# Kernel tuning notes

Hardware: AMD Instinct MI355X
Metric: run time of the kernel (lower is better)

Reference implementation:

```python
import jax, jax.numpy as jnp
import numpy as np

NUM_USER = 100000
NUM_ENT = 100000
NUM_REL = 60
NUM_ITEM = 20000
ITEM_NUM_IN_KG = 20000
DIM = 64
N_NEIGHBOR = 8
N_ITER = 2
BATCH = 16384


def setup_inputs() -> dict:
    key = jax.random.key(0)
    ks = jax.random.split(key, 10)
    return {
        "u": jax.random.randint(ks[0], (BATCH,), 0, NUM_USER),
        "v": jax.random.randint(ks[1], (BATCH,), 0, NUM_ITEM),
        "usr_emb": jax.random.normal(ks[2], (NUM_USER, DIM), jnp.float32),
        "item_emb": jax.random.normal(ks[3], (NUM_ITEM, DIM), jnp.float32),
        "ent_emb": jax.random.normal(ks[4], (NUM_ENT + 1, DIM), jnp.float32),
        "rel_emb": jax.random.normal(ks[5], (NUM_REL + 1, DIM), jnp.float32),
        "W": jax.random.normal(ks[6], (DIM, DIM), jnp.float32) / np.sqrt(DIM),
        "b": jax.random.normal(ks[7], (DIM,), jnp.float32) * 0.01,
        "adj_ent": jax.random.randint(ks[8], (NUM_ENT + 1, N_NEIGHBOR), 0, NUM_ENT + 1),
        "adj_rel": jax.random.randint(ks[9], (NUM_ENT + 1, N_NEIGHBOR), 0, NUM_REL + 1),
    }


def reference(u, v, usr_emb, item_emb, ent_emb, rel_emb, W, b, adj_ent, adj_rel):
    B = u.shape[0]
    ue = usr_emb[u]  # [B, D]

    # hop-0 indices: items not in the KG map to the padding entity for neighbor lookup
    v_clip = jnp.where(v >= ITEM_NUM_IN_KG, NUM_ENT, v)
    ents = [v_clip[:, None]]  # [B, 1]
    rels = []
    for h in range(N_ITER):
        rels.append(adj_rel[ents[h]].reshape(B, -1))  # [B, 8**(h+1)]
        ents.append(adj_ent[ents[h]].reshape(B, -1))

    # hop-0 embedding uses the ORIGINAL v via the item table (entities[0][:] = v)
    ev = [item_emb[v[:, None]]] + [ent_emb[e] for e in ents[1:]]  # each [B, m, D]
    rv = [rel_emb[r] for r in rels]

    for i in range(N_ITER):
        act = jnp.tanh if i == N_ITER - 1 else jax.nn.sigmoid
        nxt = []
        for hop in range(N_ITER - i):
            sv = ev[hop]  # [B, m, D]
            m = sv.shape[1]
            nv = ev[hop + 1].reshape(B, m, N_NEIGHBOR, DIM)
            nr = rv[hop].reshape(B, m, N_NEIGHBOR, DIM)
            # user-relation attention over the 8 sampled neighbors
            scores = jnp.einsum("bd,bmnd->bmn", ue, nr)
            wgt = jax.nn.softmax(scores, axis=-1)
            agg = jnp.einsum("bmn,bmnd->bmd", wgt, nv)
            out = (sv + agg) @ W.T + b  # 'sum' aggregator
            nxt.append(act(out))
        ev = nxt

    item_vec = ev[0].reshape(B, DIM)
    return jax.nn.sigmoid(jnp.sum(ue * item_vec, axis=1))  # [B]
```

## Files before the change

kernel.cpp:

```cpp
#include <hip/hip_runtime.h>
#include <hip/hip_fp16.h>


namespace {

constexpr int kDim      = 64;
constexpr int kNN       = 8;
constexpr int kNumEnt   = 100000;
constexpr int kItemInKG = 20000;
constexpr int kElems    = 8;
constexpr int kRelChunks = 976;
constexpr int kP        = 68;
constexpr size_t kEntHalfBytes = (size_t)(kNumEnt + 1) * kDim * sizeof(__half);

typedef _Float16 f16x4 __attribute__((ext_vector_type(4)));
typedef _Float16 f16x8 __attribute__((ext_vector_type(8)));
typedef float    f32x4 __attribute__((ext_vector_type(4)));

__device__ __forceinline__ float fast_sigmoid(float x) {
  return 1.0f / (1.0f + __expf(-x));
}
__device__ __forceinline__ float fast_tanh(float x) {
  return 2.0f / (1.0f + __expf(-2.0f * x)) - 1.0f;
}
__device__ __forceinline__ float readlane_f(float v, int lane) {
  return __int_as_float(__builtin_amdgcn_readlane(__float_as_int(v), lane));
}
__device__ __forceinline__ f16x8 join8(f16x4 lo, f16x4 hi) {
  return __builtin_shufflevector(lo, hi, 0, 1, 2, 3, 4, 5, 6, 7);
}
__device__ __forceinline__ f16x4 cvt4(float4 f) {
  f16x4 h;
  h[0] = (_Float16)f.x; h[1] = (_Float16)f.y;
  h[2] = (_Float16)f.z; h[3] = (_Float16)f.w;
  return h;
}

__global__ void __launch_bounds__(256)
conv_kernel(const float* __restrict__ src, __half2* __restrict__ dst, int n4) {
  const int i = blockIdx.x * 256 + threadIdx.x;
  if (i < n4) {
    const float4 f = reinterpret_cast<const float4*>(src)[i];
    dst[2 * i + 0] = __floats2half2_rn(f.x, f.y);
    dst[2 * i + 1] = __floats2half2_rn(f.z, f.w);
  }
}

template <bool HALF>
__global__ void __launch_bounds__(kElems * 64)
__attribute__((amdgpu_waves_per_eu(4)))
kgcn_kernel(const int* __restrict__ u, const int* __restrict__ v,
            const float* __restrict__ usr_emb, const float* __restrict__ item_emb,
            const float* __restrict__ ent_emb, const __half* __restrict__ ent_h,
            const float* __restrict__ rel_emb,
            const float* __restrict__ W, const float* __restrict__ bias,
            const int* __restrict__ adj_ent, const int* __restrict__ adj_rel,
            float* __restrict__ out)
{
  const int tid = threadIdx.x;
  const int wv  = tid >> 6;
  const int ln  = tid & 63;
  const int lq  = ln & 15;
  const int lg  = ln >> 4;
  const int b   = blockIdx.x * kElems + wv;

  __shared__ __align__(16) _Float16 s_wh[kDim * kP];
  __shared__ __align__(16) _Float16 s_relh[kDim * kP];
  __shared__ __align__(16) _Float16 s_ueh[kElems * kDim];
  __shared__ __align__(16) _Float16 s_pre[72 * kP];
  __shared__ __align__(16) _Float16 s_h[72 * kP];
  __shared__ float s_w2[kElems][kDim];

  const float4* W4 = reinterpret_cast<const float4*>(W);
  const float4* R4 = reinterpret_cast<const float4*>(rel_emb);
  const float4 wst0 = W4[tid];
  const float4 wst1 = W4[512 + tid];
  const float4 rst0 = R4[tid];
  const float4 rst1 = (512 + tid < kRelChunks) ? R4[512 + tid]
                                               : make_float4(0.f, 0.f, 0.f, 0.f);

  const int bs    = __builtin_amdgcn_readfirstlane(b);
  const int uid_s = u[bs];
  const int vid_s = v[bs];
  const int e0s   = (vid_s >= kItemInKG) ? kNumEnt : vid_s;

  const float ue  = usr_emb[(size_t)uid_s * kDim + ln];
  const float ev0 = item_emb[(size_t)vid_s * kDim + ln];

  int e1s[kNN];
  {
    const int* __restrict__ a0 = adj_ent + (size_t)e0s * kNN;
    #pragma unroll
    for (int m = 0; m < kNN; ++m) e1s[m] = a0[m];
  }
  int e2s[kDim];
  #pragma unroll
  for (int m = 0; m < kNN; ++m) {
    const int* __restrict__ am = adj_ent + (size_t)e1s[m] * kNN;
    #pragma unroll
    for (int n = 0; n < kNN; ++n) e2s[m * kNN + n] = am[n];
  }
  int r1v = 0;
  if (ln < kNN) r1v = adj_rel[(size_t)e0s * kNN + ln];
  int parent = e1s[0];
  #pragma unroll
  for (int m = 1; m < kNN; ++m)
    parent = ((ln >> 3) == m) ? e1s[m] : parent;
  const int r2v = adj_rel[(size_t)parent * kNN + (ln & 7)];

  {
    int id = tid, row = id >> 4, c4 = (id & 15) << 2;
    *reinterpret_cast<f16x4*>(&s_wh[row * kP + c4]) = cvt4(wst0);
    *reinterpret_cast<f16x4*>(&s_relh[row * kP + c4]) = cvt4(rst0);
    id = 512 + tid; row = id >> 4; c4 = (id & 15) << 2;
    *reinterpret_cast<f16x4*>(&s_wh[row * kP + c4]) = cvt4(wst1);
    *reinterpret_cast<f16x4*>(&s_relh[row * kP + c4]) = cvt4(rst1);
  }
  s_ueh[wv * kDim + ln] = (_Float16)ue;

  float ev1r[kNN];
  #pragma unroll
  for (int m = 0; m < kNN; ++m) {
    const size_t row = (size_t)e1s[m] * kDim + ln;
    ev1r[m] = HALF ? __half2float(ent_h[row]) : ent_emb[row];
  }

  unsigned short g16[kDim];
  if constexpr (HALF) {
    const unsigned short* eh = reinterpret_cast<const unsigned short*>(ent_h);
    #pragma unroll
    for (int i = 0; i < kDim; ++i)
      g16[i] = eh[(size_t)e2s[i] * kDim + ln];
  }

  __syncthreads();

  f16x8 Au[2];
  #pragma unroll
  for (int s = 0; s < 2; ++s) {
    const _Float16* p = &s_ueh[wv * kDim + s * 32 + lg * 4];
    Au[s] = join8(*reinterpret_cast<const f16x4*>(p),
                  *reinterpret_cast<const f16x4*>(p + 16));
  }
  f32x4 ts[4];
  #pragma unroll
  for (int tt = 0; tt < 4; ++tt) {
    ts[tt] = f32x4{0.f, 0.f, 0.f, 0.f};
    #pragma unroll
    for (int s = 0; s < 2; ++s) {
      const _Float16* p = &s_relh[(tt * 16 + lq) * kP + s * 32 + lg * 4];
      const f16x8 Rf = join8(*reinterpret_cast<const f16x4*>(p),
                             *reinterpret_cast<const f16x4*>(p + 16));
      ts[tt] = __builtin_amdgcn_mfma_f32_16x16x32_f16(Au[s], Rf, ts[tt],
                                                      0, 0, 0);
    }
  }
  auto t_lookup = [&](int r) -> float {
    const int sl = r & 15;
    const float c0 = __shfl(ts[0][0], sl, 64);
    const float c1 = __shfl(ts[1][0], sl, 64);
    const float c2 = __shfl(ts[2][0], sl, 64);
    const float c3 = __shfl(ts[3][0], sl, 64);
    const float ab = (r & 16) ? c1 : c0;
    const float cd = (r & 16) ? c3 : c2;
    return (r & 32) ? cd : ab;
  };

  {
    const float s2 = t_lookup(r2v);
    float mx = s2;
    #pragma unroll
    for (int m = 1; m <= 4; m <<= 1) mx = fmaxf(mx, __shfl_xor(mx, m, 64));
    const float e = __expf(s2 - mx);
    float sm = e;
    #pragma unroll
    for (int m = 1; m <= 4; m <<= 1) sm += __shfl_xor(sm, m, 64);
    s_w2[wv][ln] = e / sm;
  }
  float w0v;
  {
    const float s0 = t_lookup(r1v);
    float mx = s0;
    #pragma unroll
    for (int m = 1; m <= 4; m <<= 1) mx = fmaxf(mx, __shfl_xor(mx, m, 64));
    w0v = __expf(s0 - mx);
    float sm = w0v;
    #pragma unroll
    for (int m = 1; m <= 4; m <<= 1) sm += __shfl_xor(sm, m, 64);
    w0v /= sm;
  }

  if constexpr (HALF) {
    #pragma unroll
    for (int i = 0; i < kDim; ++i) asm volatile("" : "+v"(g16[i]));
  }

  {
    float agg = 0.f;
    #pragma unroll
    for (int n = 0; n < kNN; ++n)
      agg = fmaf(readlane_f(w0v, n), ev1r[n], agg);
    s_pre[(wv * 9 + 0) * kP + ln] = (_Float16)(ev0 + agg);
  }
  if constexpr (HALF) {
    #pragma unroll
    for (int m = 0; m < kNN; ++m) {
      float acc = 0.f;
      #pragma unroll
      for (int n = 0; n < kNN; ++n) {
        const _Float16 hv =
            __builtin_bit_cast(_Float16, g16[m * kNN + n]);
        acc = fmaf((float)hv, s_w2[wv][m * kNN + n], acc);
      }
      s_pre[(wv * 9 + 1 + m) * kP + ln] = (_Float16)(ev1r[m] + acc);
    }
  } else {
    #pragma unroll 2
    for (int m = 0; m < kNN; ++m) {
      float acc = 0.f;
      #pragma unroll
      for (int n = 0; n < kNN; ++n) {
        const size_t row = (size_t)e2s[m * kNN + n] * kDim + ln;
        acc = fmaf(s_w2[wv][m * kNN + n], ent_emb[row], acc);
      }
      s_pre[(wv * 9 + 1 + m) * kP + ln] = (_Float16)(ev1r[m] + acc);
    }
  }

  float bcol[4];
  #pragma unroll
  for (int tt = 0; tt < 4; ++tt) bcol[tt] = bias[tt * 16 + lq];

  f16x8 Bf[8];
  #pragma unroll
  for (int tt = 0; tt < 4; ++tt) {
    #pragma unroll
    for (int s = 0; s < 2; ++s) {
      const _Float16* p = &s_wh[(tt * 16 + lq) * kP + s * 32 + lg * 4];
      Bf[tt * 2 + s] = join8(*reinterpret_cast<const f16x4*>(p),
                             *reinterpret_cast<const f16x4*>(p + 16));
    }
  }

  const int arow = wv * 9 + (lq < 9 ? lq : 8);
  f16x8 Af[2];
  #pragma unroll
  for (int s = 0; s < 2; ++s) {
    const _Float16* p = &s_pre[arow * kP + s * 32 + lg * 4];
    Af[s] = join8(*reinterpret_cast<const f16x4*>(p),
                  *reinterpret_cast<const f16x4*>(p + 16));
  }
  f32x4 acc[4];
  #pragma unroll
  for (int tt = 0; tt < 4; ++tt) acc[tt] = f32x4{0.f, 0.f, 0.f, 0.f};
  #pragma unroll
  for (int tt = 0; tt < 4; ++tt)
    #pragma unroll
    for (int s = 0; s < 2; ++s)
      acc[tt] = __builtin_amdgcn_mfma_f32_16x16x32_f16(Af[s], Bf[tt * 2 + s],
                                                       acc[tt], 0, 0, 0);

  #pragma unroll
  for (int tt = 0; tt < 4; ++tt) {
    #pragma unroll
    for (int r = 0; r < 4; ++r) {
      const int vec = lg * 4 + r;
      if (vec < 9)
        s_h[(wv * 9 + vec) * kP + tt * 16 + lq] =
            (_Float16)fast_sigmoid(acc[tt][r] + bcol[tt]);
    }
  }

  {
    float pre = (float)s_h[(wv * 9 + 0) * kP + ln];
    #pragma unroll
    for (int n = 0; n < kNN; ++n)
      pre = fmaf(readlane_f(w0v, n), (float)s_h[(wv * 9 + 1 + n) * kP + ln],
                 pre);
    s_pre[(wv * 9 + 0) * kP + ln] = (_Float16)pre;
  }

  f16x8 Ff[2];
  #pragma unroll
  for (int s = 0; s < 2; ++s) {
    const _Float16* p = &s_pre[(wv * 9 + 0) * kP + s * 32 + lg * 4];
    Ff[s] = join8(*reinterpret_cast<const f16x4*>(p),
                  *reinterpret_cast<const f16x4*>(p + 16));
  }
  f32x4 fa[4];
  #pragma unroll
  for (int tt = 0; tt < 4; ++tt) fa[tt] = f32x4{0.f, 0.f, 0.f, 0.f};
  #pragma unroll
  for (int tt = 0; tt < 4; ++tt)
    #pragma unroll
    for (int s = 0; s < 2; ++s)
      fa[tt] = __builtin_amdgcn_mfma_f32_16x16x32_f16(Ff[s], Bf[tt * 2 + s],
                                                      fa[tt], 0, 0, 0);

  {
    float fown = fa[0][0], bown = bcol[0];
    if (lg == 1) { fown = fa[1][0]; bown = bcol[1]; }
    if (lg == 2) { fown = fa[2][0]; bown = bcol[2]; }
    if (lg == 3) { fown = fa[3][0]; bown = bcol[3]; }
    float part = fast_tanh(fown + bown) * ue;
    #pragma unroll
    for (int off = 32; off > 0; off >>= 1)
      part += __shfl_xor(part, off, 64);
    if (ln == 0) out[b] = fast_sigmoid(part);
  }
}

}

extern "C" void kernel_launch(void* const* d_in, const int* in_sizes, int n_in,
                              void* d_out, int out_size, void* d_ws, size_t ws_size,
                              hipStream_t stream) {
  const int*   u        = (const int*)d_in[0];
  const int*   v        = (const int*)d_in[1];
  const float* usr_emb  = (const float*)d_in[2];
  const float* item_emb = (const float*)d_in[3];
  const float* ent_emb  = (const float*)d_in[4];
  const float* rel_emb  = (const float*)d_in[5];
  const float* W        = (const float*)d_in[6];
  const float* bias     = (const float*)d_in[7];
  const int*   adj_ent  = (const int*)d_in[8];
  const int*   adj_rel  = (const int*)d_in[9];
  float*       out      = (float*)d_out;

  const int B = in_sizes[0];
  dim3 grid(B / kElems), block(kElems * 64);

  const bool use_half = (ws_size >= kEntHalfBytes);
  if (use_half) {
    __half* ent_h = (__half*)d_ws;
    const int n4 = (kNumEnt + 1) * kDim / 4;
    hipLaunchKernelGGL(conv_kernel, dim3((n4 + 255) / 256), dim3(256), 0,
                       stream, ent_emb, (__half2*)ent_h, n4);
    hipLaunchKernelGGL((kgcn_kernel<true>), grid, block, 0, stream,
                       u, v, usr_emb, item_emb, ent_emb, ent_h, rel_emb, W,
                       bias, adj_ent, adj_rel, out);
  } else {
    hipLaunchKernelGGL((kgcn_kernel<false>), grid, block, 0, stream,
                       u, v, usr_emb, item_emb, ent_emb, (const __half*)d_ws,
                       rel_emb, W, bias, adj_ent, adj_rel, out);
  }
}
```

Measured before the change: 52.26 us.

## Process two batch elements per wave with software-pipelined gathers

Each wave now handles two batch elements, and the grid is halved. Index and embedding gathers for the second element are issued while the first element's attention and MLP math runs, so memory latency is hidden and the per-block staging of W and relation tables is amortized. The cost is many more live registers (two 64-entry gather arrays), which may cut occupancy or cause spills, and fewer blocks in flight.

Measured after the change: 103.6 us. 98.3% more time.

```diff
diff --git a/kernel.cpp b/kernel.cpp
--- a/kernel.cpp
+++ b/kernel.cpp
@@ -9,6 +9,7 @@
 constexpr int kNumEnt   = 100000;
 constexpr int kItemInKG = 20000;
 constexpr int kElems    = 8;
+constexpr int kEPW      = 2;
 constexpr int kRelChunks = 976;
 constexpr int kP        = 68;
 constexpr size_t kEntHalfBytes = (size_t)(kNumEnt + 1) * kDim * sizeof(__half);
@@ -62,7 +63,8 @@
   const int ln  = tid & 63;
   const int lq  = ln & 15;
   const int lg  = ln >> 4;
-  const int b   = blockIdx.x * kElems + wv;
+  const int b0  = blockIdx.x * (kElems * kEPW) + wv;
+  const int b1  = b0 + kElems;
 
   __shared__ __align__(16) _Float16 s_wh[kDim * kP];
   __shared__ __align__(16) _Float16 s_relh[kDim * kP];
@@ -79,34 +81,44 @@
   const float4 rst1 = (512 + tid < kRelChunks) ? R4[512 + tid]
                                                : make_float4(0.f, 0.f, 0.f, 0.f);
 
-  const int bs    = __builtin_amdgcn_readfirstlane(b);
-  const int uid_s = u[bs];
-  const int vid_s = v[bs];
-  const int e0s   = (vid_s >= kItemInKG) ? kNumEnt : vid_s;
-
-  const float ue  = usr_emb[(size_t)uid_s * kDim + ln];
-  const float ev0 = item_emb[(size_t)vid_s * kDim + ln];
-
-  int e1s[kNN];
-  {
-    const int* __restrict__ a0 = adj_ent + (size_t)e0s * kNN;
-    #pragma unroll
-    for (int m = 0; m < kNN; ++m) e1s[m] = a0[m];
-  }
-  int e2s[kDim];
+  const int bs0   = __builtin_amdgcn_readfirstlane(b0);
+  const int uid0  = u[bs0];
+  const int vid0  = v[bs0];
+  const int e0s0  = (vid0 >= kItemInKG) ? kNumEnt : vid0;
+  const float ue0  = usr_emb[(size_t)uid0 * kDim + ln];
+  const float ev00 = item_emb[(size_t)vid0 * kDim + ln];
+
+  int e1s0[kNN];
+  {
+    const int* __restrict__ a0 = adj_ent + (size_t)e0s0 * kNN;
+    #pragma unroll
+    for (int m = 0; m < kNN; ++m) e1s0[m] = a0[m];
+  }
+  int e2s0[kDim];
   #pragma unroll
   for (int m = 0; m < kNN; ++m) {
-    const int* __restrict__ am = adj_ent + (size_t)e1s[m] * kNN;
-    #pragma unroll
-    for (int n = 0; n < kNN; ++n) e2s[m * kNN + n] = am[n];
-  }
-  int r1v = 0;
-  if (ln < kNN) r1v = adj_rel[(size_t)e0s * kNN + ln];
-  int parent = e1s[0];
+    const int* __restrict__ am = adj_ent + (size_t)e1s0[m] * kNN;
+    #pragma unroll
+    for (int n = 0; n < kNN; ++n) e2s0[m * kNN + n] = am[n];
+  }
+  int r1v0 = 0;
+  if (ln < kNN) r1v0 = adj_rel[(size_t)e0s0 * kNN + ln];
+  int parent0 = e1s0[0];
   #pragma unroll
   for (int m = 1; m < kNN; ++m)
-    parent = ((ln >> 3) == m) ? e1s[m] : parent;
-  const int r2v = adj_rel[(size_t)parent * kNN + (ln & 7)];
+    parent0 = ((ln >> 3) == m) ? e1s0[m] : parent0;
+  const int r2v0 = adj_rel[(size_t)parent0 * kNN + (ln & 7)];
+
+  const int bs1   = __builtin_amdgcn_readfirstlane(b1);
+  const int uid1  = u[bs1];
+  const int vid1  = v[bs1];
+  const int e0s1  = (vid1 >= kItemInKG) ? kNumEnt : vid1;
+  int e1s1[kNN];
+  {
+    const int* __restrict__ a1 = adj_ent + (size_t)e0s1 * kNN;
+    #pragma unroll
+    for (int m = 0; m < kNN; ++m) e1s1[m] = a1[m];
+  }
 
   {
     int id = tid, row = id >> 4, c4 = (id & 15) << 2;
@@ -116,91 +128,123 @@
     *reinterpret_cast<f16x4*>(&s_wh[row * kP + c4]) = cvt4(wst1);
     *reinterpret_cast<f16x4*>(&s_relh[row * kP + c4]) = cvt4(rst1);
   }
-  s_ueh[wv * kDim + ln] = (_Float16)ue;
-
-  float ev1r[kNN];
+  s_ueh[wv * kDim + ln] = (_Float16)ue0;
+
+  float ev1r0[kNN];
   #pragma unroll
   for (int m = 0; m < kNN; ++m) {
-    const size_t row = (size_t)e1s[m] * kDim + ln;
-    ev1r[m] = HALF ? __half2float(ent_h[row]) : ent_emb[row];
-  }
-
-  unsigned short g16[kDim];
+    const size_t row = (size_t)e1s0[m] * kDim + ln;
+    ev1r0[m] = HALF ? __half2float(ent_h[row]) : ent_emb[row];
+  }
+  unsigned short g16_0[kDim];
   if constexpr (HALF) {
     const unsigned short* eh = reinterpret_cast<const unsigned short*>(ent_h);
     #pragma unroll
     for (int i = 0; i < kDim; ++i)
-      g16[i] = eh[(size_t)e2s[i] * kDim + ln];
-  }
+      g16_0[i] = eh[(size_t)e2s0[i] * kDim + ln];
+  }
+
+  int e2s1[kDim];
+  #pragma unroll
+  for (int m = 0; m < kNN; ++m) {
+    const int* __restrict__ am = adj_ent + (size_t)e1s1[m] * kNN;
+    #pragma unroll
+    for (int n = 0; n < kNN; ++n) e2s1[m * kNN + n] = am[n];
+  }
+  int r1v1 = 0;
+  if (ln < kNN) r1v1 = adj_rel[(size_t)e0s1 * kNN + ln];
+  int parent1 = e1s1[0];
+  #pragma unroll
+  for (int m = 1; m < kNN; ++m)
+    parent1 = ((ln >> 3) == m) ? e1s1[m] : parent1;
+  const int r2v1 = adj_rel[(size_t)parent1 * kNN + (ln & 7)];
 
   __syncthreads();
 
-  f16x8 Au[2];
-  #pragma unroll
-  for (int s = 0; s < 2; ++s) {
-    const _Float16* p = &s_ueh[wv * kDim + s * 32 + lg * 4];
-    Au[s] = join8(*reinterpret_cast<const f16x4*>(p),
-                  *reinterpret_cast<const f16x4*>(p + 16));
-  }
-  f32x4 ts[4];
-  #pragma unroll
-  for (int tt = 0; tt < 4; ++tt) {
-    ts[tt] = f32x4{0.f, 0.f, 0.f, 0.f};
-    #pragma unroll
-    for (int s = 0; s < 2; ++s) {
-      const _Float16* p = &s_relh[(tt * 16 + lq) * kP + s * 32 + lg * 4];
-      const f16x8 Rf = join8(*reinterpret_cast<const f16x4*>(p),
-                             *reinterpret_cast<const f16x4*>(p + 16));
-      ts[tt] = __builtin_amdgcn_mfma_f32_16x16x32_f16(Au[s], Rf, ts[tt],
-                                                      0, 0, 0);
-    }
-  }
-  auto t_lookup = [&](int r) -> float {
-    const int sl = r & 15;
-    const float c0 = __shfl(ts[0][0], sl, 64);
-    const float c1 = __shfl(ts[1][0], sl, 64);
-    const float c2 = __shfl(ts[2][0], sl, 64);
-    const float c3 = __shfl(ts[3][0], sl, 64);
-    const float ab = (r & 16) ? c1 : c0;
-    const float cd = (r & 16) ? c3 : c2;
-    return (r & 32) ? cd : ab;
-  };
-
-  {
-    const float s2 = t_lookup(r2v);
-    float mx = s2;
-    #pragma unroll
-    for (int m = 1; m <= 4; m <<= 1) mx = fmaxf(mx, __shfl_xor(mx, m, 64));
-    const float e = __expf(s2 - mx);
-    float sm = e;
-    #pragma unroll
-    for (int m = 1; m <= 4; m <<= 1) sm += __shfl_xor(sm, m, 64);
-    s_w2[wv][ln] = e / sm;
-  }
-  float w0v;
-  {
-    const float s0 = t_lookup(r1v);
-    float mx = s0;
-    #pragma unroll
-    for (int m = 1; m <= 4; m <<= 1) mx = fmaxf(mx, __shfl_xor(mx, m, 64));
-    w0v = __expf(s0 - mx);
-    float sm = w0v;
-    #pragma unroll
-    for (int m = 1; m <= 4; m <<= 1) sm += __shfl_xor(sm, m, 64);
-    w0v /= sm;
+  float w0v0, w2v_unused0;
+  {
+    f16x8 Au[2];
+    #pragma unroll
+    for (int s = 0; s < 2; ++s) {
+      const _Float16* p = &s_ueh[wv * kDim + s * 32 + lg * 4];
+      Au[s] = join8(*reinterpret_cast<const f16x4*>(p),
+                    *reinterpret_cast<const f16x4*>(p + 16));
+    }
+    f32x4 ts[4];
+    #pragma unroll
+    for (int tt = 0; tt < 4; ++tt) {
+      ts[tt] = f32x4{0.f, 0.f, 0.f, 0.f};
+      #pragma unroll
+      for (int s = 0; s < 2; ++s) {
+        const _Float16* p = &s_relh[(tt * 16 + lq) * kP + s * 32 + lg * 4];
+        const f16x8 Rf = join8(*reinterpret_cast<const f16x4*>(p),
+                               *reinterpret_cast<const f16x4*>(p + 16));
+        ts[tt] = __builtin_amdgcn_mfma_f32_16x16x32_f16(Au[s], Rf, ts[tt],
+                                                        0, 0, 0);
+      }
+    }
+    auto t_lookup = [&](int r) -> float {
+      const int sl = r & 15;
+      const float c0 = __shfl(ts[0][0], sl, 64);
+      const float c1 = __shfl(ts[1][0], sl, 64);
+      const float c2 = __shfl(ts[2][0], sl, 64);
+      const float c3 = __shfl(ts[3][0], sl, 64);
+      const float ab = (r & 16) ? c1 : c0;
+      const float cd = (r & 16) ? c3 : c2;
+      return (r & 32) ? cd : ab;
+    };
+    {
+      const float s2 = t_lookup(r2v0);
+      float mx = s2;
+      #pragma unroll
+      for (int m = 1; m <= 4; m <<= 1) mx = fmaxf(mx, __shfl_xor(mx, m, 64));
+      const float e = __expf(s2 - mx);
+      float sm = e;
+      #pragma unroll
+      for (int m = 1; m <= 4; m <<= 1) sm += __shfl_xor(sm, m, 64);
+      s_w2[wv][ln] = e / sm;
+    }
+    {
+      const float s0 = t_lookup(r1v0);
+      float mx = s0;
+      #pragma unroll
+      for (int m = 1; m <= 4; m <<= 1) mx = fmaxf(mx, __shfl_xor(mx, m, 64));
+      w0v0 = __expf(s0 - mx);
+      float sm = w0v0;
+      #pragma unroll
+      for (int m = 1; m <= 4; m <<= 1) sm += __shfl_xor(sm, m, 64);
+      w0v0 /= sm;
+    }
+    (void)w2v_unused0;
   }
 
   if constexpr (HALF) {
     #pragma unroll
-    for (int i = 0; i < kDim; ++i) asm volatile("" : "+v"(g16[i]));
+    for (int i = 0; i < kDim; ++i) asm volatile("" : "+v"(g16_0[i]));
+  }
+
+  const float ue1  = usr_emb[(size_t)uid1 * kDim + ln];
+  const float ev01 = item_emb[(size_t)vid1 * kDim + ln];
+  float ev1r1[kNN];
+  #pragma unroll
+  for (int m = 0; m < kNN; ++m) {
+    const size_t row = (size_t)e1s1[m] * kDim + ln;
+    ev1r1[m] = HALF ? __half2float(ent_h[row]) : ent_emb[row];
+  }
+  unsigned short g16_1[kDim];
+  if constexpr (HALF) {
+    const unsigned short* eh = reinterpret_cast<const unsigned short*>(ent_h);
+    #pragma unroll
+    for (int i = 0; i < kDim; ++i)
+      g16_1[i] = eh[(size_t)e2s1[i] * kDim + ln];
   }
 
   {
     float agg = 0.f;
     #pragma unroll
     for (int n = 0; n < kNN; ++n)
-      agg = fmaf(readlane_f(w0v, n), ev1r[n], agg);
-    s_pre[(wv * 9 + 0) * kP + ln] = (_Float16)(ev0 + agg);
+      agg = fmaf(readlane_f(w0v0, n), ev1r0[n], agg);
+    s_pre[(wv * 9 + 0) * kP + ln] = (_Float16)(ev00 + agg);
   }
   if constexpr (HALF) {
     #pragma unroll
@@ -208,11 +252,10 @@
       float acc = 0.f;
       #pragma unroll
       for (int n = 0; n < kNN; ++n) {
-        const _Float16 hv =
-            __builtin_bit_cast(_Float16, g16[m * kNN + n]);
+        const _Float16 hv = __builtin_bit_cast(_Float16, g16_0[m * kNN + n]);
         acc = fmaf((float)hv, s_w2[wv][m * kNN + n], acc);
       }
-      s_pre[(wv * 9 + 1 + m) * kP + ln] = (_Float16)(ev1r[m] + acc);
+      s_pre[(wv * 9 + 1 + m) * kP + ln] = (_Float16)(ev1r0[m] + acc);
     }
   } else {
     #pragma unroll 2
@@ -220,17 +263,16 @@
       float acc = 0.f;
       #pragma unroll
       for (int n = 0; n < kNN; ++n) {
-        const size_t row = (size_t)e2s[m * kNN + n] * kDim + ln;
+        const size_t row = (size_t)e2s0[m * kNN + n] * kDim + ln;
         acc = fmaf(s_w2[wv][m * kNN + n], ent_emb[row], acc);
       }
-      s_pre[(wv * 9 + 1 + m) * kP + ln] = (_Float16)(ev1r[m] + acc);
+      s_pre[(wv * 9 + 1 + m) * kP + ln] = (_Float16)(ev1r0[m] + acc);
     }
   }
 
   float bcol[4];
   #pragma unroll
   for (int tt = 0; tt < 4; ++tt) bcol[tt] = bias[tt * 16 + lq];
-
   f16x8 Bf[8];
   #pragma unroll
   for (int tt = 0; tt < 4; ++tt) {
@@ -241,72 +283,223 @@
                              *reinterpret_cast<const f16x4*>(p + 16));
     }
   }
-
   const int arow = wv * 9 + (lq < 9 ? lq : 8);
-  f16x8 Af[2];
-  #pragma unroll
-  for (int s = 0; s < 2; ++s) {
-    const _Float16* p = &s_pre[arow * kP + s * 32 + lg * 4];
-    Af[s] = join8(*reinterpret_cast<const f16x4*>(p),
-                  *reinterpret_cast<const f16x4*>(p + 16));
-  }
-  f32x4 acc[4];
-  #pragma unroll
-  for (int tt = 0; tt < 4; ++tt) acc[tt] = f32x4{0.f, 0.f, 0.f, 0.f};
-  #pragma unroll
-  for (int tt = 0; tt < 4; ++tt)
-    #pragma unroll
-    for (int s = 0; s < 2; ++s)
-      acc[tt] = __builtin_amdgcn_mfma_f32_16x16x32_f16(Af[s], Bf[tt * 2 + s],
-                                                       acc[tt], 0, 0, 0);
-
-  #pragma unroll
-  for (int tt = 0; tt < 4; ++tt) {
-    #pragma unroll
-    for (int r = 0; r < 4; ++r) {
-      const int vec = lg * 4 + r;
-      if (vec < 9)
-        s_h[(wv * 9 + vec) * kP + tt * 16 + lq] =
-            (_Float16)fast_sigmoid(acc[tt][r] + bcol[tt]);
-    }
-  }
-
-  {
-    float pre = (float)s_h[(wv * 9 + 0) * kP + ln];
-    #pragma unroll
-    for (int n = 0; n < kNN; ++n)
-      pre = fmaf(readlane_f(w0v, n), (float)s_h[(wv * 9 + 1 + n) * kP + ln],
-                 pre);
-    s_pre[(wv * 9 + 0) * kP + ln] = (_Float16)pre;
-  }
-
-  f16x8 Ff[2];
-  #pragma unroll
-  for (int s = 0; s < 2; ++s) {
-    const _Float16* p = &s_pre[(wv * 9 + 0) * kP + s * 32 + lg * 4];
-    Ff[s] = join8(*reinterpret_cast<const f16x4*>(p),
-                  *reinterpret_cast<const f16x4*>(p + 16));
-  }
-  f32x4 fa[4];
-  #pragma unroll
-  for (int tt = 0; tt < 4; ++tt) fa[tt] = f32x4{0.f, 0.f, 0.f, 0.f};
-  #pragma unroll
-  for (int tt = 0; tt < 4; ++tt)
-    #pragma unroll
-    for (int s = 0; s < 2; ++s)
-      fa[tt] = __builtin_amdgcn_mfma_f32_16x16x32_f16(Ff[s], Bf[tt * 2 + s],
-                                                      fa[tt], 0, 0, 0);
-
-  {
+
+  {
+    f16x8 Af[2];
+    #pragma unroll
+    for (int s = 0; s < 2; ++s) {
+      const _Float16* p = &s_pre[arow * kP + s * 32 + lg * 4];
+      Af[s] = join8(*reinterpret_cast<const f16x4*>(p),
+                    *reinterpret_cast<const f16x4*>(p + 16));
+    }
+    f32x4 acc[4];
+    #pragma unroll
+    for (int tt = 0; tt < 4; ++tt) acc[tt] = f32x4{0.f, 0.f, 0.f, 0.f};
+    #pragma unroll
+    for (int tt = 0; tt < 4; ++tt)
+      #pragma unroll
+      for (int s = 0; s < 2; ++s)
+        acc[tt] = __builtin_amdgcn_mfma_f32_16x16x32_f16(Af[s], Bf[tt * 2 + s],
+                                                         acc[tt], 0, 0, 0);
+    #pragma unroll
+    for (int tt = 0; tt < 4; ++tt) {
+      #pragma unroll
+      for (int r = 0; r < 4; ++r) {
+        const int vec = lg * 4 + r;
+        if (vec < 9)
+          s_h[(wv * 9 + vec) * kP + tt * 16 + lq] =
+              (_Float16)fast_sigmoid(acc[tt][r] + bcol[tt]);
+      }
+    }
+    {
+      float pre = (float)s_h[(wv * 9 + 0) * kP + ln];
+      #pragma unroll
+      for (int n = 0; n < kNN; ++n)
+        pre = fmaf(readlane_f(w0v0, n),
+                   (float)s_h[(wv * 9 + 1 + n) * kP + ln], pre);
+      s_pre[(wv * 9 + 0) * kP + ln] = (_Float16)pre;
+    }
+    f16x8 Ff[2];
+    #pragma unroll
+    for (int s = 0; s < 2; ++s) {
+      const _Float16* p = &s_pre[(wv * 9 + 0) * kP + s * 32 + lg * 4];
+      Ff[s] = join8(*reinterpret_cast<const f16x4*>(p),
+                    *reinterpret_cast<const f16x4*>(p + 16));
+    }
+    f32x4 fa[4];
+    #pragma unroll
+    for (int tt = 0; tt < 4; ++tt) fa[tt] = f32x4{0.f, 0.f, 0.f, 0.f};
+    #pragma unroll
+    for (int tt = 0; tt < 4; ++tt)
+      #pragma unroll
+      for (int s = 0; s < 2; ++s)
+        fa[tt] = __builtin_amdgcn_mfma_f32_16x16x32_f16(Ff[s], Bf[tt * 2 + s],
+                                                        fa[tt], 0, 0, 0);
     float fown = fa[0][0], bown = bcol[0];
     if (lg == 1) { fown = fa[1][0]; bown = bcol[1]; }
     if (lg == 2) { fown = fa[2][0]; bown = bcol[2]; }
     if (lg == 3) { fown = fa[3][0]; bown = bcol[3]; }
-    float part = fast_tanh(fown + bown) * ue;
+    float part = fast_tanh(fown + bown) * ue0;
     #pragma unroll
     for (int off = 32; off > 0; off >>= 1)
       part += __shfl_xor(part, off, 64);
-    if (ln == 0) out[b] = fast_sigmoid(part);
+    if (ln == 0) out[b0] = fast_sigmoid(part);
+  }
+
+  s_ueh[wv * kDim + ln] = (_Float16)ue1;
+  float w0v1;
+  {
+    f16x8 Au[2];
+    #pragma unroll
+    for (int s = 0; s < 2; ++s) {
+      const _Float16* p = &s_ueh[wv * kDim + s * 32 + lg * 4];
+      Au[s] = join8(*reinterpret_cast<const f16x4*>(p),
+                    *reinterpret_cast<const f16x4*>(p + 16));
+    }
+    f32x4 ts[4];
+    #pragma unroll
+    for (int tt = 0; tt < 4; ++tt) {
+      ts[tt] = f32x4{0.f, 0.f, 0.f, 0.f};
+      #pragma unroll
+      for (int s = 0; s < 2; ++s) {
+        const _Float16* p = &s_relh[(tt * 16 + lq) * kP + s * 32 + lg * 4];
+        const f16x8 Rf = join8(*reinterpret_cast<const f16x4*>(p),
+                               *reinterpret_cast<const f16x4*>(p + 16));
+        ts[tt] = __builtin_amdgcn_mfma_f32_16x16x32_f16(Au[s], Rf, ts[tt],
+                                                        0, 0, 0);
+      }
+    }
+    auto t_lookup = [&](int r) -> float {
+      const int sl = r & 15;
+      const float c0 = __shfl(ts[0][0], sl, 64);
+      const float c1 = __shfl(ts[1][0], sl, 64);
+      const float c2 = __shfl(ts[2][0], sl, 64);
+      const float c3 = __shfl(ts[3][0], sl, 64);
+      const float ab = (r & 16) ? c1 : c0;
+      const float cd = (r & 16) ? c3 : c2;
+      return (r & 32) ? cd : ab;
+    };
+    {
+      const float s2 = t_lookup(r2v1);
+      float mx = s2;
+      #pragma unroll
+      for (int m = 1; m <= 4; m <<= 1) mx = fmaxf(mx, __shfl_xor(mx, m, 64));
+      const float e = __expf(s2 - mx);
+      float sm = e;
+      #pragma unroll
+      for (int m = 1; m <= 4; m <<= 1) sm += __shfl_xor(sm, m, 64);
+      s_w2[wv][ln] = e / sm;
+    }
+    {
+      const float s0 = t_lookup(r1v1);
+      float mx = s0;
+      #pragma unroll
+      for (int m = 1; m <= 4; m <<= 1) mx = fmaxf(mx, __shfl_xor(mx, m, 64));
+      w0v1 = __expf(s0 - mx);
+      float sm = w0v1;
+      #pragma unroll
+      for (int m = 1; m <= 4; m <<= 1) sm += __shfl_xor(sm, m, 64);
+      w0v1 /= sm;
+    }
+  }
+
+  if constexpr (HALF) {
+    #pragma unroll
+    for (int i = 0; i < kDim; ++i) asm volatile("" : "+v"(g16_1[i]));
+  }
+
+  {
+    float agg = 0.f;
+    #pragma unroll
+    for (int n = 0; n < kNN; ++n)
+      agg = fmaf(readlane_f(w0v1, n), ev1r1[n], agg);
+    s_pre[(wv * 9 + 0) * kP + ln] = (_Float16)(ev01 + agg);
+  }
+  if constexpr (HALF) {
+    #pragma unroll
+    for (int m = 0; m < kNN; ++m) {
+      float acc = 0.f;
+      #pragma unroll
+      for (int n = 0; n < kNN; ++n) {
+        const _Float16 hv = __builtin_bit_cast(_Float16, g16_1[m * kNN + n]);
+        acc = fmaf((float)hv, s_w2[wv][m * kNN + n], acc);
+      }
+      s_pre[(wv * 9 + 1 + m) * kP + ln] = (_Float16)(ev1r1[m] + acc);
+    }
+  } else {
+    #pragma unroll 2
+    for (int m = 0; m < kNN; ++m) {
+      float acc = 0.f;
+      #pragma unroll
+      for (int n = 0; n < kNN; ++n) {
+        const size_t row = (size_t)e2s1[m * kNN + n] * kDim + ln;
+        acc = fmaf(s_w2[wv][m * kNN + n], ent_emb[row], acc);
+      }
+      s_pre[(wv * 9 + 1 + m) * kP + ln] = (_Float16)(ev1r1[m] + acc);
+    }
+  }
+
+  {
+    f16x8 Af[2];
+    #pragma unroll
+    for (int s = 0; s < 2; ++s) {
+      const _Float16* p = &s_pre[arow * kP + s * 32 + lg * 4];
+      Af[s] = join8(*reinterpret_cast<const f16x4*>(p),
+                    *reinterpret_cast<const f16x4*>(p + 16));
+    }
+    f32x4 acc[4];
+    #pragma unroll
+    for (int tt = 0; tt < 4; ++tt) acc[tt] = f32x4{0.f, 0.f, 0.f, 0.f};
+    #pragma unroll
+    for (int tt = 0; tt < 4; ++tt)
+      #pragma unroll
+      for (int s = 0; s < 2; ++s)
+        acc[tt] = __builtin_amdgcn_mfma_f32_16x16x32_f16(Af[s], Bf[tt * 2 + s],
+                                                         acc[tt], 0, 0, 0);
+    #pragma unroll
+    for (int tt = 0; tt < 4; ++tt) {
+      #pragma unroll
+      for (int r = 0; r < 4; ++r) {
+        const int vec = lg * 4 + r;
+        if (vec < 9)
+          s_h[(wv * 9 + vec) * kP + tt * 16 + lq] =
+              (_Float16)fast_sigmoid(acc[tt][r] + bcol[tt]);
+      }
+    }
+    {
+      float pre = (float)s_h[(wv * 9 + 0) * kP + ln];
+      #pragma unroll
+      for (int n = 0; n < kNN; ++n)
+        pre = fmaf(readlane_f(w0v1, n),
+                   (float)s_h[(wv * 9 + 1 + n) * kP + ln], pre);
+      s_pre[(wv * 9 + 0) * kP + ln] = (_Float16)pre;
+    }
+    f16x8 Ff[2];
+    #pragma unroll
+    for (int s = 0; s < 2; ++s) {
+      const _Float16* p = &s_pre[(wv * 9 + 0) * kP + s * 32 + lg * 4];
+      Ff[s] = join8(*reinterpret_cast<const f16x4*>(p),
+                    *reinterpret_cast<const f16x4*>(p + 16));
+    }
+    f32x4 fa[4];
+    #pragma unroll
+    for (int tt = 0; tt < 4; ++tt) fa[tt] = f32x4{0.f, 0.f, 0.f, 0.f};
+    #pragma unroll
+    for (int tt = 0; tt < 4; ++tt)
+      #pragma unroll
+      for (int s = 0; s < 2; ++s)
+        fa[tt] = __builtin_amdgcn_mfma_f32_16x16x32_f16(Ff[s], Bf[tt * 2 + s],
+                                                        fa[tt], 0, 0, 0);
+    float fown = fa[0][0], bown = bcol[0];
+    if (lg == 1) { fown = fa[1][0]; bown = bcol[1]; }
+    if (lg == 2) { fown = fa[2][0]; bown = bcol[2]; }
+    if (lg == 3) { fown = fa[3][0]; bown = bcol[3]; }
+    float part = fast_tanh(fown + bown) * ue1;
+    #pragma unroll
+    for (int off = 32; off > 0; off >>= 1)
+      part += __shfl_xor(part, off, 64);
+    if (ln == 0) out[b1] = fast_sigmoid(part);
   }
 }
 
@@ -328,7 +521,7 @@
   float*       out      = (float*)d_out;
 
   const int B = in_sizes[0];
-  dim3 grid(B / kElems), block(kElems * 64);
+  dim3 grid(B / (kElems * kEPW)), block(kElems * 64);
 
   const bool use_half = (ws_size >= kEntHalfBytes);
   if (use_half) {
```
